# Kernel tuning notes

Hardware: AMD Instinct MI355X
Metric: run time of the kernel (lower is better)

Reference implementation:

```python
import jax, jax.numpy as jnp
import numpy as np
from jax import lax

N_NODES = 100000
N_EDGES = 1600000
NUM_GRAPHS = 2000
F_IN = 64
HIDDEN = 64
NUM_LAYERS = 3
K = 7
NUM_CLASSES = 10


def setup_inputs() -> dict:
    key = jax.random.key(0)
    ks = jax.random.split(key, 16)
    x = jax.random.normal(ks[0], (N_NODES, F_IN), jnp.float32)
    edge_index = jax.random.randint(ks[1], (2, N_EDGES), 0, N_NODES)
    batch = jnp.sort(jax.random.randint(ks[2], (N_NODES,), 0, NUM_GRAPHS))
    s = 1.0 / np.sqrt(HIDDEN)
    p = lambda k_, sh: jax.random.uniform(k_, sh, jnp.float32, -s, s)
    return dict(
        x=x, edge_index=edge_index, batch=batch,
        W1l=p(ks[3], (F_IN, HIDDEN)), b1=p(ks[4], (HIDDEN,)), W1r=p(ks[5], (F_IN, HIDDEN)),
        W2l=p(ks[6], (HIDDEN, HIDDEN)), b2=p(ks[7], (HIDDEN,)), W2r=p(ks[8], (HIDDEN, HIDDEN)),
        W3l=p(ks[9], (HIDDEN, HIDDEN)), b3=p(ks[10], (HIDDEN,)), W3r=p(ks[11], (HIDDEN, HIDDEN)),
        conv1d_w=p(ks[12], (32, HIDDEN, NUM_LAYERS)), conv1d_b=jnp.zeros((32,), jnp.float32),
        lin1_w=p(ks[13], (32 * (K - NUM_LAYERS + 1), HIDDEN)), lin1_b=jnp.zeros((HIDDEN,), jnp.float32),
        lin2_w=p(ks[14], (HIDDEN, NUM_CLASSES)), lin2_b=jnp.zeros((NUM_CLASSES,), jnp.float32),
    )


def _sage(x, src, dst, Wl, b, Wr):
    # PyG SAGEConv (aggr='mean'): lin_l(mean_j x_j) + lin_r(x_i); lin_l carries the bias.
    n = x.shape[0]
    msum = jax.ops.segment_sum(x[src], dst, num_segments=n)          # [N, D] gather+scatter
    cnt = jax.ops.segment_sum(jnp.ones((src.shape[0],), x.dtype), dst, num_segments=n)
    mean = msum / jnp.maximum(cnt, 1.0)[:, None]
    return mean @ Wl + b + x @ Wr


def _sort_pool(x, batch, num_graphs, k):
    # SortAggregation: per graph, sort nodes descending by last feature channel,
    # keep top-k, zero-pad short graphs, flatten to [B, k*D].
    N, D = x.shape
    perm = jnp.lexsort((-x[:, -1], batch))  # primary: graph id, secondary: desc last channel
    sb = batch[perm]
    counts = jax.ops.segment_sum(jnp.ones((N,), jnp.int32), batch, num_segments=num_graphs)
    starts = jnp.concatenate([jnp.zeros((1,), jnp.int32), jnp.cumsum(counts)[:-1]])
    rank = jnp.arange(N, dtype=jnp.int32) - starts[sb]
    valid = rank < k
    b_idx = jnp.where(valid, sb, num_graphs)  # route overflow nodes to dummy row
    r_idx = jnp.where(valid, rank, 0)
    out = jnp.zeros((num_graphs + 1, k, D), x.dtype).at[b_idx, r_idx].set(x[perm])
    return out[:num_graphs].reshape(num_graphs, k * D)


def reference(x, edge_index, batch, W1l, b1, W1r, W2l, b2, W2r, W3l, b3, W3r,
              conv1d_w, conv1d_b, lin1_w, lin1_b, lin2_w, lin2_b):
    src, dst = edge_index[0], edge_index[1]
    h = jax.nn.relu(_sage(x, src, dst, W1l, b1, W1r))
    h = jax.nn.relu(_sage(h, src, dst, W2l, b2, W2r))
    h = jax.nn.relu(_sage(h, src, dst, W3l, b3, W3r))
    g = _sort_pool(h, batch, NUM_GRAPHS, K)                       # [B, K*H]
    g = g.reshape(NUM_GRAPHS, K, HIDDEN).transpose(0, 2, 1)       # [B, H, K]
    c = lax.conv_general_dilated(g, conv1d_w, (1,), 'VALID',
                                 dimension_numbers=('NCH', 'OIH', 'NCH'))
    c = jax.nn.relu(c + conv1d_b[None, :, None])                  # [B, 32, K-ks+1]
    flat = c.reshape(NUM_GRAPHS, -1)
    h1 = jax.nn.relu(flat @ lin1_w + lin1_b)                      # dropout = identity (eval)
    logits = h1 @ lin2_w + lin2_b
    return jax.nn.log_softmax(logits, axis=-1)
```

## Files before the change

### kernel.cpp

```cpp
#include <hip/hip_runtime.h>
#include <hip/hip_bf16.h>

#define NN 100000
#define NE 1600000
#define NG 2000
#define KTOP 7

#define BNODES 128
#define NBKT 782
#define EPB 8192
#define NL1B 196
#define L2CAP 4096

#define GEMM_BLOCKS 768
#define NTILES 1563
#define SMEM_FLOATS (64 * 68 + 2 * 64 * 64)

#define ACC4(A, V) do { A.x += V.x; A.y += V.y; A.z += V.z; A.w += V.w; } while (0)
#define ACC4P(A, U, W) do { A.x += U.x + W.x; A.y += U.y + W.y; \
                            A.z += U.z + W.z; A.w += U.w + W.w; } while (0)

__device__ __forceinline__ void agg_node(const float* __restrict__ XLp, const int* __restrict__ ce,
        int s, int e, int fo, float4& a0, float4& a1, float4& a2, float4& a3) {
    int a = s;
    for (; a + 2 <= e; a += 2) {
        const float4* p0 = (const float4*)(XLp + ((size_t)ce[a] << 6) + fo);
        const float4* p1 = (const float4*)(XLp + ((size_t)ce[a + 1] << 6) + fo);
        float4 u0 = p0[0], u1 = p0[1], u2 = p0[2], u3 = p0[3];
        float4 w0 = p1[0], w1 = p1[1], w2 = p1[2], w3 = p1[3];
        ACC4P(a0, u0, w0); ACC4P(a1, u1, w1); ACC4P(a2, u2, w2); ACC4P(a3, u3, w3);
    }
    if (a < e) {
        const float4* p0 = (const float4*)(XLp + ((size_t)ce[a] << 6) + fo);
        float4 u0 = p0[0], u1 = p0[1], u2 = p0[2], u3 = p0[3];
        ACC4(a0, u0); ACC4(a1, u1); ACC4(a2, u2); ACC4(a3, u3);
    }
}

__device__ __forceinline__ void relu_mean_res(float inv, const float4* tp,
        float4& h0, float4& h1, float4& h2, float4& h3) {
    float4 t0 = tp[0], t1 = tp[1], t2 = tp[2], t3 = tp[3];
    h0.x = fmaxf(h0.x * inv + t0.x, 0.f); h0.y = fmaxf(h0.y * inv + t0.y, 0.f);
    h0.z = fmaxf(h0.z * inv + t0.z, 0.f); h0.w = fmaxf(h0.w * inv + t0.w, 0.f);
    h1.x = fmaxf(h1.x * inv + t1.x, 0.f); h1.y = fmaxf(h1.y * inv + t1.y, 0.f);
    h1.z = fmaxf(h1.z * inv + t1.z, 0.f); h1.w = fmaxf(h1.w * inv + t1.w, 0.f);
    h2.x = fmaxf(h2.x * inv + t2.x, 0.f); h2.y = fmaxf(h2.y * inv + t2.y, 0.f);
    h2.z = fmaxf(h2.z * inv + t2.z, 0.f); h2.w = fmaxf(h2.w * inv + t2.w, 0.f);
    h3.x = fmaxf(h3.x * inv + t3.x, 0.f); h3.y = fmaxf(h3.y * inv + t3.y, 0.f);
    h3.z = fmaxf(h3.z * inv + t3.z, 0.f); h3.w = fmaxf(h3.w * inv + t3.w, 0.f);
}

#define FMA4C(av, B, acc) do { \
    acc[0] = fmaf(av, B.x, acc[0]); acc[1] = fmaf(av, B.y, acc[1]); \
    acc[2] = fmaf(av, B.z, acc[2]); acc[3] = fmaf(av, B.w, acc[3]); } while (0)

__device__ __forceinline__ void gemm_tile(const float* As, const float* Bl, const float* Br,
        int n0, int ty4, int tx4, float b0, float b1v, float b2v, float b3v,
        float* __restrict__ XL, float* __restrict__ T,
        float* __restrict__ kc_out, float* __restrict__ tc_out) {
    float accl[4][4] = {{0.f}}, accr[4][4] = {{0.f}};
    for (int kc = 0; kc < 64; kc += 4) {
        float4 Av[4], L[4], R[4];
        #pragma unroll
        for (int i = 0; i < 4; ++i) Av[i] = *(const float4*)&As[(ty4 + i) * 68 + kc];
        #pragma unroll
        for (int j = 0; j < 4; ++j) {
            L[j] = *(const float4*)&Bl[(kc + j) * 64 + tx4];
            R[j] = *(const float4*)&Br[(kc + j) * 64 + tx4];
        }
        #pragma unroll
        for (int i = 0; i < 4; ++i) {
            FMA4C(Av[i].x, L[0], accl[i]); FMA4C(Av[i].y, L[1], accl[i]);
            FMA4C(Av[i].z, L[2], accl[i]); FMA4C(Av[i].w, L[3], accl[i]);
            FMA4C(Av[i].x, R[0], accr[i]); FMA4C(Av[i].y, R[1], accr[i]);
            FMA4C(Av[i].z, R[2], accr[i]); FMA4C(Av[i].w, R[3], accr[i]);
        }
    }
    #pragma unroll
    for (int i = 0; i < 4; ++i) {
        int g = n0 + ty4 + i;
        if (g < NN) {
            *(float4*)&XL[(size_t)g * 64 + tx4] =
                make_float4(accl[i][0], accl[i][1], accl[i][2], accl[i][3]);
            *(float4*)&T[(size_t)g * 64 + tx4] =
                make_float4(accr[i][0] + b0, accr[i][1] + b1v, accr[i][2] + b2v, accr[i][3] + b3v);
            if (kc_out && tx4 == 60) {
                kc_out[g] = accl[i][3];
                tc_out[g] = accr[i][3] + b3v;
            }
        }
    }
}

__device__ __forceinline__ void stage_weights(float* Bl, float* Br,
        const float* __restrict__ Wl, const float* __restrict__ Wr, int t) {
    #pragma unroll
    for (int q = 0; q < 4; ++q) {
        int idx = t + q * 256;
        ((float4*)Bl)[idx] = ((const float4*)Wl)[idx];
        ((float4*)Br)[idx] = ((const float4*)Wr)[idx];
    }
}

__device__ __forceinline__ void gemm_body(int bid, int nblocks, float* smem,
        const float* __restrict__ X, const float* __restrict__ Wl,
        const float* __restrict__ Wr, const float* __restrict__ bias,
        float* __restrict__ XL, float* __restrict__ T) {
    float* As = smem;
    float* Bl = smem + 64 * 68;
    float* Br = Bl + 64 * 64;
    int t = threadIdx.x;
    stage_weights(Bl, Br, Wl, Wr, t);
    int ty4 = (t >> 4) * 4, tx4 = (t & 15) * 4;
    float b0 = bias[tx4 + 0], b1v = bias[tx4 + 1], b2v = bias[tx4 + 2], b3v = bias[tx4 + 3];
    for (int tile = bid; tile < NTILES; tile += nblocks) {
        int n0 = tile * 64;
        #pragma unroll
        for (int q = 0; q < 4; ++q) {
            int f = t + q * 256;
            int node = f >> 4, seg = f & 15;
            int g = n0 + node;
            float4 v = make_float4(0.f, 0.f, 0.f, 0.f);
            if (g < NN) v = *(const float4*)&X[(size_t)g * 64 + seg * 4];
            *(float4*)&As[node * 68 + seg * 4] = v;
        }
        __syncthreads();
        gemm_tile(As, Bl, Br, n0, ty4, tx4, b0, b1v, b2v, b3v, XL, T, nullptr, nullptr);
        __syncthreads();
    }
}

__global__ __launch_bounds__(256) void k_aggemm(const float* __restrict__ XL_in,
        float* __restrict__ T, const int* __restrict__ ptr, const int* __restrict__ ce,
        const float* __restrict__ Wl, const float* __restrict__ Wr,
        const float* __restrict__ bias, float* __restrict__ XL_out,
        float* __restrict__ kc_out, float* __restrict__ tc_out) {
    __shared__ float smem[SMEM_FLOATS];
    float* As = smem;
    float* Bl = smem + 64 * 68;
    float* Br = Bl + 64 * 64;
    int t = threadIdx.x;
    stage_weights(Bl, Br, Wl, Wr, t);
    int node_l = t >> 2;
    int fo = (t & 3) * 16;
    int ty4 = (t >> 4) * 4, tx4 = (t & 15) * 4;
    float b0 = bias[tx4 + 0], b1v = bias[tx4 + 1], b2v = bias[tx4 + 2], b3v = bias[tx4 + 3];
    for (int tile = blockIdx.x; tile < NTILES; tile += GEMM_BLOCKS) {
        int n0 = tile * 64;
        int i = n0 + node_l;
        float4 h0 = make_float4(0.f, 0.f, 0.f, 0.f), h1 = h0, h2 = h0, h3 = h0;
        if (i < NN) {
            int s = ptr[i], e = ptr[i + 1];
            agg_node(XL_in, ce, s, e, fo, h0, h1, h2, h3);
            float inv = 1.f / fmaxf((float)(e - s), 1.f);
            relu_mean_res(inv, (const float4*)(T + ((size_t)i << 6) + fo), h0, h1, h2, h3);
        }
        float* dst = &As[node_l * 68 + fo];
        ((float4*)dst)[0] = h0; ((float4*)dst)[1] = h1;
        ((float4*)dst)[2] = h2; ((float4*)dst)[3] = h3;
        __syncthreads();
        gemm_tile(As, Bl, Br, n0, ty4, tx4, b0, b1v, b2v, b3v, XL_out, T, kc_out, tc_out);
        __syncthreads();
    }
}

__global__ __launch_bounds__(256) void k_key(const float* __restrict__ keycol,
        const float* __restrict__ tcol, const int* __restrict__ ptr,
        const int* __restrict__ ce, float* __restrict__ key) {
    int i = blockIdx.x * 256 + threadIdx.x;
    if (i >= NN) return;
    int s = ptr[i], e = ptr[i + 1];
    float acc = 0.f;
    int a = s;
    for (; a + 2 <= e; a += 2) acc += keycol[ce[a]] + keycol[ce[a + 1]];
    if (a < e) acc += keycol[ce[a]];
    float inv = 1.f / fmaxf((float)(e - s), 1.f);
    key[i] = fmaxf(acc * inv + tcol[i], 0.f);
}

__global__ __launch_bounds__(256) void k_topk(const float* __restrict__ key,
        const int* __restrict__ gstart, int* __restrict__ idx7, int G) {
    int wv = threadIdx.x >> 6, lane = threadIdx.x & 63;
    int b = blockIdx.x * 4 + wv;
    if (b >= G) return;
    int s = gstart[b], e = gstart[b + 1];
    float pk = 3.4e38f; int pi = -1;
    for (int r = 0; r < KTOP; ++r) {
        float bk = -1.f; int bi = -1;
        for (int i = s + lane; i < e; i += 64) {
            float k = key[i];
            bool elig = (k < pk) || (k == pk && i > pi);
            if (elig && (k > bk || (k == bk && (unsigned)i < (unsigned)bi))) { bk = k; bi = i; }
        }
        #pragma unroll
        for (int off = 1; off < 64; off <<= 1) {
            float ok = __shfl_xor(bk, off);
            int   oi = __shfl_xor(bi, off);
            if (ok > bk || (ok == bk && (unsigned)oi < (unsigned)bi)) { bk = ok; bi = oi; }
        }
        if (lane == 0) idx7[b * KTOP + r] = bi;
        pk = bk; pi = bi;
    }
}

__global__ __launch_bounds__(256) void k_aggW(const float* __restrict__ XL_in,
        const float* __restrict__ T, const int* __restrict__ ptr, const int* __restrict__ ce,
        const int* __restrict__ idx7, float* __restrict__ H3W) {
    int t = threadIdx.x;
    int j = blockIdx.x * 64 + (t >> 2);
    int fo = (t & 3) * 16;
    if (j >= NG * KTOP) return;
    int i = idx7[j];
    float4 h0 = make_float4(0.f, 0.f, 0.f, 0.f), h1 = h0, h2 = h0, h3 = h0;
    if (i >= 0) {
        int s = ptr[i], e = ptr[i + 1];
        agg_node(XL_in, ce, s, e, fo, h0, h1, h2, h3);
        float inv = 1.f / fmaxf((float)(e - s), 1.f);
        relu_mean_res(inv, (const float4*)(T + ((size_t)i << 6) + fo), h0, h1, h2, h3);
    }
    float4* dst = (float4*)(H3W + (size_t)j * 64 + fo);
    dst[0] = h0; dst[1] = h1; dst[2] = h2; dst[3] = h3;
}

__global__ __launch_bounds__(256) void k_front(const float* __restrict__ X,
        const float* __restrict__ Wl, const float* __restrict__ Wr,
        const float* __restrict__ bias, float* __restrict__ XL, float* __restrict__ T,
        const int* __restrict__ edst, int* __restrict__ bh,
        const int* __restrict__ bat, int* __restrict__ gstart) {
    __shared__ float smem[SMEM_FLOATS];
    int bid = blockIdx.x, t = threadIdx.x;
    if (bid < GEMM_BLOCKS) {
        gemm_body(bid, GEMM_BLOCKS, smem, X, Wl, Wr, bias, XL, T);
    } else if (bid < GEMM_BLOCKS + NL1B) {
        int bk = bid - GEMM_BLOCKS;
        int* h = (int*)smem;
        for (int q = t; q < NBKT; q += 256) h[q] = 0;
        __syncthreads();
        int e0 = bk * EPB, e1 = min(e0 + EPB, NE);
        for (int e = e0 + t; e < e1; e += 256) atomicAdd(&h[edst[e] >> 7], 1);
        __syncthreads();
        for (int q = t; q < NBKT; q += 256) bh[bk * NBKT + q] = h[q];
    } else {
        int g = (bid - GEMM_BLOCKS - NL1B) * 256 + t;
        if (g <= NG) {
            int lo = 0, hi = NN;
            while (lo < hi) { int mid = (lo + hi) >> 1; if (bat[mid] < g) lo = mid + 1; else hi = mid; }
            gstart[g] = lo;
        }
    }
}

__global__ void k_colscan(int* __restrict__ bh, int* __restrict__ btot) {
    __shared__ int carry;
    int b = blockIdx.x, t = threadIdx.x;
    if (t == 0) carry = 0;
    __syncthreads();
    for (int base = 0; base < NL1B; base += 64) {
        int idx = base + t;
        int v = (idx < NL1B) ? bh[idx * NBKT + b] : 0;
        int x = v;
        #pragma unroll
        for (int off = 1; off < 64; off <<= 1) {
            int y = __shfl_up(x, off);
            if (t >= off) x += y;
        }
        int c = carry;
        if (idx < NL1B) bh[idx * NBKT + b] = c + x - v;
        __syncthreads();
        if (t == 63) carry = c + x;
        __syncthreads();
    }
    if (t == 0) btot[b] = carry;
}

__global__ void k_btscan(const int* __restrict__ btot, int* __restrict__ bstart) {
    __shared__ int s[1024];
    int t = threadIdx.x;
    int v = (t < NBKT) ? btot[t] : 0;
    s[t] = v; __syncthreads();
    for (int off = 1; off < 1024; off <<= 1) {
        int y = (t >= off) ? s[t - off] : 0;
        __syncthreads();
        s[t] += y;
        __syncthreads();
    }
    if (t < NBKT) bstart[t] = s[t] - v;
    if (t == NBKT - 1) bstart[NBKT] = s[t];
}

__global__ __launch_bounds__(256) void k_bscatter(const int* __restrict__ esrc,
        const int* __restrict__ edst, const int* __restrict__ bh,
        const int* __restrict__ bstart, int* __restrict__ ebuf) {
    __shared__ int cur[NBKT];
    int t = threadIdx.x, bk = blockIdx.x;
    for (int q = t; q < NBKT; q += 256) cur[q] = bstart[q] + bh[bk * NBKT + q];
    __syncthreads();
    int e0 = bk * EPB, e1 = min(e0 + EPB, NE);
    for (int e = e0 + t; e < e1; e += 256) {
        int d = edst[e], s = esrc[e];
        int pos = atomicAdd(&cur[d >> 7], 1);
        ebuf[pos] = s | ((d & 127) << 20);
    }
}

__global__ __launch_bounds__(128) void k_bbuild(const int* __restrict__ ebuf,
        const int* __restrict__ bstart, int* __restrict__ ce, int* __restrict__ ptr) {
    __shared__ int lord[L2CAP];
    __shared__ int cnt[BNODES], sc[BNODES], cursor[BNODES];
    int b = blockIdx.x, t = threadIdx.x;
    int base = bstart[b], nb = bstart[b + 1] - base;
    cnt[t] = 0;
    __syncthreads();
    for (int j = t; j < nb; j += 128) atomicAdd(&cnt[ebuf[base + j] >> 20], 1);
    __syncthreads();
    int v = cnt[t]; sc[t] = v; __syncthreads();
    for (int off = 1; off < 128; off <<= 1) {
        int y = (t >= off) ? sc[t - off] : 0;
        __syncthreads();
        sc[t] += y;
        __syncthreads();
    }
    int segend = sc[t], segstart = sc[t] - v;
    cursor[t] = segstart;
    __syncthreads();
    bool fits = (nb <= L2CAP);
    for (int j = t; j < nb; j += 128) {
        int pv = ebuf[base + j];
        int node = pv >> 20;
        int pos = atomicAdd(&cursor[node], 1);
        if (fits) lord[pos] = pv & 0xFFFFF;
        else ce[base + pos] = pv & 0xFFFFF;
    }
    __syncthreads();
    if (fits) {
        for (int a = segstart + 1; a < segend; ++a) {
            int val = lord[a]; int j = a - 1;
            while (j >= segstart && lord[j] > val) { lord[j + 1] = lord[j]; --j; }
            lord[j + 1] = val;
        }
        __syncthreads();
        for (int j = t; j < nb; j += 128) ce[base + j] = lord[j];
    } else {
        for (int a = segstart + 1; a < segend; ++a) {
            int val = ce[base + a]; int j = a - 1;
            while (j >= segstart && ce[base + j] > val) { ce[base + j + 1] = ce[base + j]; --j; }
            ce[base + j + 1] = val;
        }
    }
    int node = b * BNODES + t;
    if (node <= NN) ptr[node] = base + segstart;
}

__global__ __launch_bounds__(256) void k_head(const float* __restrict__ H3W,
        const float* __restrict__ cw, const float* __restrict__ cb,
        const float* __restrict__ l1w, const float* __restrict__ l1b,
        const float* __restrict__ l2w, const float* __restrict__ l2b,
        float* __restrict__ out, int G) {
    __shared__ float sw[32 * 64 * 3];
    __shared__ float s2w[64 * 10];
    __shared__ float sg[4][KTOP][64];
    __shared__ float sflat[4][160];
    __shared__ float sh1[4][64];
    __shared__ float slog[4][10];
    int t = threadIdx.x;
    for (int q = t; q < 32 * 64 * 3; q += 256) sw[q] = cw[q];
    for (int q = t; q < 640; q += 256) s2w[q] = l2w[q];
    int wv = t >> 6, lane = t & 63;
    int b = blockIdx.x * 4 + wv;
    for (int r = 0; r < KTOP; ++r)
        sg[wv][r][lane] = H3W[(size_t)(b * KTOP + r) * 64 + lane];
    __syncthreads();
    for (int idx = lane; idx < 160; idx += 64) {
        int o = idx / 5, p = idx % 5;
        float acc = cb[o];
        #pragma unroll
        for (int dt = 0; dt < 3; ++dt) {
            const float* wrow = &sw[(o * 64) * 3 + dt];
            const float* grow = &sg[wv][p + dt][0];
            for (int i = 0; i < 64; ++i) acc = fmaf(wrow[i * 3], grow[i], acc);
        }
        sflat[wv][idx] = fmaxf(acc, 0.f);
    }
    __syncthreads();
    {
        float acc = l1b[lane];
        for (int k = 0; k < 160; ++k) acc = fmaf(sflat[wv][k], l1w[k * 64 + lane], acc);
        sh1[wv][lane] = fmaxf(acc, 0.f);
    }
    __syncthreads();
    if (lane < 10) {
        float acc = l2b[lane];
        for (int k = 0; k < 64; ++k) acc = fmaf(sh1[wv][k], s2w[k * 10 + lane], acc);
        slog[wv][lane] = acc;
    }
    __syncthreads();
    if (lane < 10) {
        float m = -3.4e38f;
        for (int j = 0; j < 10; ++j) m = fmaxf(m, slog[wv][j]);
        float ssum = 0.f;
        for (int j = 0; j < 10; ++j) ssum += expf(slog[wv][j] - m);
        out[b * 10 + lane] = slog[wv][lane] - m - logf(ssum);
    }
}

extern "C" void kernel_launch(void* const* d_in, const int* in_sizes, int n_in,
                              void* d_out, int out_size, void* d_ws, size_t ws_size,
                              hipStream_t stream) {
    const float* x   = (const float*)d_in[0];
    const int*   ei  = (const int*)d_in[1];
    const int*   bat = (const int*)d_in[2];
    const float* W1l = (const float*)d_in[3], *b1 = (const float*)d_in[4], *W1r = (const float*)d_in[5];
    const float* W2l = (const float*)d_in[6], *b2 = (const float*)d_in[7], *W2r = (const float*)d_in[8];
    const float* W3l = (const float*)d_in[9], *b3 = (const float*)d_in[10], *W3r = (const float*)d_in[11];
    const float* cw  = (const float*)d_in[12], *cb  = (const float*)d_in[13];
    const float* l1w = (const float*)d_in[14], *l1b = (const float*)d_in[15];
    const float* l2w = (const float*)d_in[16], *l2b = (const float*)d_in[17];
    float* out = (float*)d_out;
    const int* esrc = ei;
    const int* edst = ei + NE;

    char* w = (char*)d_ws;
    size_t off = 0;
    auto take = [&](size_t bytes) { void* p = w + off; off = (off + bytes + 255) & ~(size_t)255; return p; };
    int*   bh      = (int*)take((size_t)NL1B * NBKT * 4);
    int*   btot    = (int*)take((size_t)NBKT * 4);
    int*   bstart  = (int*)take((size_t)(NBKT + 1) * 4);
    int*   gstart  = (int*)take((size_t)(NG + 1) * 4);
    int*   idx7    = (int*)take((size_t)NG * KTOP * 4);
    int*   ebuf    = (int*)take((size_t)NE * 4);
    int*   csr_ptr = (int*)take((size_t)(NN + 1) * 4);
    int*   csr_e   = (int*)take((size_t)NE * 4);
    float* XLa     = (float*)take((size_t)NN * 64 * 4);
    float* XLb     = (float*)take((size_t)NN * 64 * 4);
    float* T       = (float*)take((size_t)NN * 64 * 4);
    float* keycol  = (float*)take((size_t)NN * 4);
    float* tcol    = (float*)take((size_t)NN * 4);
    float* key     = (float*)take((size_t)NN * 4);
    float* H3W     = (float*)take((size_t)NG * KTOP * 64 * 4);

    k_front<<<GEMM_BLOCKS + NL1B + 8, 256, 0, stream>>>(x, W1l, W1r, b1, XLa, T,
                                                        edst, bh, bat, gstart);
    k_colscan<<<NBKT, 64, 0, stream>>>(bh, btot);
    k_btscan <<<1, 1024, 0, stream>>>(btot, bstart);
    k_bscatter<<<NL1B, 256, 0, stream>>>(esrc, edst, bh, bstart, ebuf);
    k_bbuild <<<NBKT, 128, 0, stream>>>(ebuf, bstart, csr_e, csr_ptr);

    k_aggemm<<<GEMM_BLOCKS, 256, 0, stream>>>(XLa, T, csr_ptr, csr_e, W2l, W2r, b2, XLb,
                                              nullptr, nullptr);
    k_aggemm<<<GEMM_BLOCKS, 256, 0, stream>>>(XLb, T, csr_ptr, csr_e, W3l, W3r, b3, XLa,
                                              keycol, tcol);

    k_key <<<(NN + 255) / 256, 256, 0, stream>>>(keycol, tcol, csr_ptr, csr_e, key);
    k_topk<<<(NG + 3) / 4, 256, 0, stream>>>(key, gstart, idx7, NG);
    k_aggW<<<(NG * KTOP + 63) / 64, 256, 0, stream>>>(XLa, T, csr_ptr, csr_e, idx7, H3W);
    k_head<<<NG / 4, 256, 0, stream>>>(H3W, cw, cb, l1w, l1b, l2w, l2b, out, NG);
}
```

Baseline: 330.1 us.

## Fuse key, top-k, gather and head into one tail kernel; drop bucket-scan kernel

Merges the key computation, per-graph top-k selection, aggregation of the selected nodes and the classifier head into a single per-graph kernel. Keys are cached in shared memory up to a capacity and recomputed beyond it. The bucket histogram is stored transposed so the column scan reads contiguously. The separate bucket-total scan kernel is removed: the scatter kernel does the exclusive scan itself, and the build kernel reduces its own prefix. This cuts four launches and the intermediate key and H3W buffers. In exchange it adds redundant prefix work in every block and serial per-graph work in the tail.

```diff
diff --git a/kernel.cpp b/kernel.cpp
--- a/kernel.cpp
+++ b/kernel.cpp
@@ -5,6 +5,7 @@
 #define NE 1600000
 #define NG 2000
 #define KTOP 7
+#define KCAP 192
 
 #define BNODES 128
 #define NBKT 782
@@ -48,6 +49,18 @@
     h2.z = fmaxf(h2.z * inv + t2.z, 0.f); h2.w = fmaxf(h2.w * inv + t2.w, 0.f);
     h3.x = fmaxf(h3.x * inv + t3.x, 0.f); h3.y = fmaxf(h3.y * inv + t3.y, 0.f);
     h3.z = fmaxf(h3.z * inv + t3.z, 0.f); h3.w = fmaxf(h3.w * inv + t3.w, 0.f);
+}
+
+__device__ __forceinline__ float compute_key(int i, const float* __restrict__ keycol,
+        const float* __restrict__ tcol, const int* __restrict__ ptr,
+        const int* __restrict__ ce) {
+    int s = ptr[i], e = ptr[i + 1];
+    float acc = 0.f;
+    int a = s;
+    for (; a + 2 <= e; a += 2) acc += keycol[ce[a]] + keycol[ce[a + 1]];
+    if (a < e) acc += keycol[ce[a]];
+    float inv = 1.f / fmaxf((float)(e - s), 1.f);
+    return fmaxf(acc * inv + tcol[i], 0.f);
 }
 
 #define FMA4C(av, B, acc) do { \
@@ -164,68 +177,10 @@
     }
 }
 
-__global__ __launch_bounds__(256) void k_key(const float* __restrict__ keycol,
-        const float* __restrict__ tcol, const int* __restrict__ ptr,
-        const int* __restrict__ ce, float* __restrict__ key) {
-    int i = blockIdx.x * 256 + threadIdx.x;
-    if (i >= NN) return;
-    int s = ptr[i], e = ptr[i + 1];
-    float acc = 0.f;
-    int a = s;
-    for (; a + 2 <= e; a += 2) acc += keycol[ce[a]] + keycol[ce[a + 1]];
-    if (a < e) acc += keycol[ce[a]];
-    float inv = 1.f / fmaxf((float)(e - s), 1.f);
-    key[i] = fmaxf(acc * inv + tcol[i], 0.f);
-}
-
-__global__ __launch_bounds__(256) void k_topk(const float* __restrict__ key,
-        const int* __restrict__ gstart, int* __restrict__ idx7, int G) {
-    int wv = threadIdx.x >> 6, lane = threadIdx.x & 63;
-    int b = blockIdx.x * 4 + wv;
-    if (b >= G) return;
-    int s = gstart[b], e = gstart[b + 1];
-    float pk = 3.4e38f; int pi = -1;
-    for (int r = 0; r < KTOP; ++r) {
-        float bk = -1.f; int bi = -1;
-        for (int i = s + lane; i < e; i += 64) {
-            float k = key[i];
-            bool elig = (k < pk) || (k == pk && i > pi);
-            if (elig && (k > bk || (k == bk && (unsigned)i < (unsigned)bi))) { bk = k; bi = i; }
-        }
-        #pragma unroll
-        for (int off = 1; off < 64; off <<= 1) {
-            float ok = __shfl_xor(bk, off);
-            int   oi = __shfl_xor(bi, off);
-            if (ok > bk || (ok == bk && (unsigned)oi < (unsigned)bi)) { bk = ok; bi = oi; }
-        }
-        if (lane == 0) idx7[b * KTOP + r] = bi;
-        pk = bk; pi = bi;
-    }
-}
-
-__global__ __launch_bounds__(256) void k_aggW(const float* __restrict__ XL_in,
-        const float* __restrict__ T, const int* __restrict__ ptr, const int* __restrict__ ce,
-        const int* __restrict__ idx7, float* __restrict__ H3W) {
-    int t = threadIdx.x;
-    int j = blockIdx.x * 64 + (t >> 2);
-    int fo = (t & 3) * 16;
-    if (j >= NG * KTOP) return;
-    int i = idx7[j];
-    float4 h0 = make_float4(0.f, 0.f, 0.f, 0.f), h1 = h0, h2 = h0, h3 = h0;
-    if (i >= 0) {
-        int s = ptr[i], e = ptr[i + 1];
-        agg_node(XL_in, ce, s, e, fo, h0, h1, h2, h3);
-        float inv = 1.f / fmaxf((float)(e - s), 1.f);
-        relu_mean_res(inv, (const float4*)(T + ((size_t)i << 6) + fo), h0, h1, h2, h3);
-    }
-    float4* dst = (float4*)(H3W + (size_t)j * 64 + fo);
-    dst[0] = h0; dst[1] = h1; dst[2] = h2; dst[3] = h3;
-}
-
 __global__ __launch_bounds__(256) void k_front(const float* __restrict__ X,
         const float* __restrict__ Wl, const float* __restrict__ Wr,
         const float* __restrict__ bias, float* __restrict__ XL, float* __restrict__ T,
-        const int* __restrict__ edst, int* __restrict__ bh,
+        const int* __restrict__ edst, int* __restrict__ bh_t,
         const int* __restrict__ bat, int* __restrict__ gstart) {
     __shared__ float smem[SMEM_FLOATS];
     int bid = blockIdx.x, t = threadIdx.x;
@@ -239,7 +194,7 @@
         int e0 = bk * EPB, e1 = min(e0 + EPB, NE);
         for (int e = e0 + t; e < e1; e += 256) atomicAdd(&h[edst[e] >> 7], 1);
         __syncthreads();
-        for (int q = t; q < NBKT; q += 256) bh[bk * NBKT + q] = h[q];
+        for (int q = t; q < NBKT; q += 256) bh_t[q * NL1B + bk] = h[q];
     } else {
         int g = (bid - GEMM_BLOCKS - NL1B) * 256 + t;
         if (g <= NG) {
@@ -250,14 +205,14 @@
     }
 }
 
-__global__ void k_colscan(int* __restrict__ bh, int* __restrict__ btot) {
+__global__ void k_colscan(int* __restrict__ bh_t, int* __restrict__ btot) {
     __shared__ int carry;
     int b = blockIdx.x, t = threadIdx.x;
     if (t == 0) carry = 0;
     __syncthreads();
     for (int base = 0; base < NL1B; base += 64) {
         int idx = base + t;
-        int v = (idx < NL1B) ? bh[idx * NBKT + b] : 0;
+        int v = (idx < NL1B) ? bh_t[b * NL1B + idx] : 0;
         int x = v;
         #pragma unroll
         for (int off = 1; off < 64; off <<= 1) {
@@ -265,7 +220,7 @@
             if (t >= off) x += y;
         }
         int c = carry;
-        if (idx < NL1B) bh[idx * NBKT + b] = c + x - v;
+        if (idx < NL1B) bh_t[b * NL1B + idx] = c + x - v;
         __syncthreads();
         if (t == 63) carry = c + x;
         __syncthreads();
@@ -273,27 +228,31 @@
     if (t == 0) btot[b] = carry;
 }
 
-__global__ void k_btscan(const int* __restrict__ btot, int* __restrict__ bstart) {
-    __shared__ int s[1024];
-    int t = threadIdx.x;
-    int v = (t < NBKT) ? btot[t] : 0;
-    s[t] = v; __syncthreads();
-    for (int off = 1; off < 1024; off <<= 1) {
-        int y = (t >= off) ? s[t - off] : 0;
-        __syncthreads();
-        s[t] += y;
-        __syncthreads();
-    }
-    if (t < NBKT) bstart[t] = s[t] - v;
-    if (t == NBKT - 1) bstart[NBKT] = s[t];
-}
-
 __global__ __launch_bounds__(256) void k_bscatter(const int* __restrict__ esrc,
-        const int* __restrict__ edst, const int* __restrict__ bh,
-        const int* __restrict__ bstart, int* __restrict__ ebuf) {
+        const int* __restrict__ edst, const int* __restrict__ bh_t,
+        const int* __restrict__ btot, int* __restrict__ ebuf) {
+    __shared__ int sbt[1024];
+    __shared__ int ssum[256];
     __shared__ int cur[NBKT];
     int t = threadIdx.x, bk = blockIdx.x;
-    for (int q = t; q < NBKT; q += 256) cur[q] = bstart[q] + bh[bk * NBKT + q];
+    for (int q = t; q < 1024; q += 256) sbt[q] = (q < NBKT) ? btot[q] : 0;
+    __syncthreads();
+    int base = t * 4;
+    int a0 = sbt[base], a1 = sbt[base + 1], a2 = sbt[base + 2], a3 = sbt[base + 3];
+    int s1 = a0 + a1, s2 = s1 + a2, s3 = s2 + a3;
+    ssum[t] = s3;
+    __syncthreads();
+    for (int off = 1; off < 256; off <<= 1) {
+        int y = (t >= off) ? ssum[t - off] : 0;
+        __syncthreads();
+        ssum[t] += y;
+        __syncthreads();
+    }
+    int prev = (t > 0) ? ssum[t - 1] : 0;
+    sbt[base] = prev; sbt[base + 1] = prev + a0;
+    sbt[base + 2] = prev + s1; sbt[base + 3] = prev + s2;
+    __syncthreads();
+    for (int q = t; q < NBKT; q += 256) cur[q] = sbt[q] + bh_t[q * NL1B + bk];
     __syncthreads();
     int e0 = bk * EPB, e1 = min(e0 + EPB, NE);
     for (int e = e0 + t; e < e1; e += 256) {
@@ -304,11 +263,21 @@
 }
 
 __global__ __launch_bounds__(128) void k_bbuild(const int* __restrict__ ebuf,
-        const int* __restrict__ bstart, int* __restrict__ ce, int* __restrict__ ptr) {
+        const int* __restrict__ btot, int* __restrict__ ce, int* __restrict__ ptr) {
     __shared__ int lord[L2CAP];
     __shared__ int cnt[BNODES], sc[BNODES], cursor[BNODES];
+    __shared__ int red[128];
     int b = blockIdx.x, t = threadIdx.x;
-    int base = bstart[b], nb = bstart[b + 1] - base;
+    int part = 0;
+    for (int j = t; j < b; j += 128) part += btot[j];
+    red[t] = part;
+    __syncthreads();
+    for (int off = 64; off >= 1; off >>= 1) {
+        if (t < off) red[t] += red[t + off];
+        __syncthreads();
+    }
+    int base = red[0];
+    int nb = btot[b];
     cnt[t] = 0;
     __syncthreads();
     for (int j = t; j < nb; j += 128) atomicAdd(&cnt[ebuf[base + j] >> 20], 1);
@@ -351,7 +320,10 @@
     if (node <= NN) ptr[node] = base + segstart;
 }
 
-__global__ __launch_bounds__(256) void k_head(const float* __restrict__ H3W,
+__global__ __launch_bounds__(256) void k_tail(const int* __restrict__ gstart,
+        const float* __restrict__ keycol, const float* __restrict__ tcol,
+        const int* __restrict__ ptr, const int* __restrict__ ce,
+        const float* __restrict__ XLa, const float* __restrict__ T,
         const float* __restrict__ cw, const float* __restrict__ cb,
         const float* __restrict__ l1w, const float* __restrict__ l1b,
         const float* __restrict__ l2w, const float* __restrict__ l2b,
@@ -362,13 +334,53 @@
     __shared__ float sflat[4][160];
     __shared__ float sh1[4][64];
     __shared__ float slog[4][10];
+    __shared__ float skey[4][KCAP];
+    __shared__ int   widx[4][KTOP];
     int t = threadIdx.x;
     for (int q = t; q < 32 * 64 * 3; q += 256) sw[q] = cw[q];
     for (int q = t; q < 640; q += 256) s2w[q] = l2w[q];
     int wv = t >> 6, lane = t & 63;
     int b = blockIdx.x * 4 + wv;
-    for (int r = 0; r < KTOP; ++r)
-        sg[wv][r][lane] = H3W[(size_t)(b * KTOP + r) * 64 + lane];
+    int s = gstart[b], e = gstart[b + 1];
+    int cnt = e - s;
+    for (int base = 0; base < cnt; base += 64) {
+        int o = base + lane;
+        if (o < cnt && o < KCAP) skey[wv][o] = compute_key(s + o, keycol, tcol, ptr, ce);
+    }
+    {
+        float pk = 3.4e38f; int pi = -1;
+        for (int r = 0; r < KTOP; ++r) {
+            float bk = -1.f; int bi = -1;
+            for (int o = lane; o < cnt; o += 64) {
+                int i = s + o;
+                float k = (o < KCAP) ? skey[wv][o] : compute_key(i, keycol, tcol, ptr, ce);
+                bool elig = (k < pk) || (k == pk && i > pi);
+                if (elig && (k > bk || (k == bk && (unsigned)i < (unsigned)bi))) { bk = k; bi = i; }
+            }
+            #pragma unroll
+            for (int off = 1; off < 64; off <<= 1) {
+                float ok = __shfl_xor(bk, off);
+                int   oi = __shfl_xor(bi, off);
+                if (ok > bk || (ok == bk && (unsigned)oi < (unsigned)bi)) { bk = ok; bi = oi; }
+            }
+            if (lane == 0) widx[wv][r] = bi;
+            pk = bk; pi = bi;
+        }
+    }
+    if (lane < 28) {
+        int r = lane >> 2, fo = (lane & 3) * 16;
+        int i = widx[wv][r];
+        float4 h0 = make_float4(0.f, 0.f, 0.f, 0.f), h1 = h0, h2 = h0, h3 = h0;
+        if (i >= 0) {
+            int s2 = ptr[i], e2 = ptr[i + 1];
+            agg_node(XLa, ce, s2, e2, fo, h0, h1, h2, h3);
+            float inv = 1.f / fmaxf((float)(e2 - s2), 1.f);
+            relu_mean_res(inv, (const float4*)(T + ((size_t)i << 6) + fo), h0, h1, h2, h3);
+        }
+        float* dstp = &sg[wv][r][fo];
+        ((float4*)dstp)[0] = h0; ((float4*)dstp)[1] = h1;
+        ((float4*)dstp)[2] = h2; ((float4*)dstp)[3] = h3;
+    }
     __syncthreads();
     for (int idx = lane; idx < 160; idx += 64) {
         int o = idx / 5, p = idx % 5;
@@ -422,11 +434,9 @@
     char* w = (char*)d_ws;
     size_t off = 0;
     auto take = [&](size_t bytes) { void* p = w + off; off = (off + bytes + 255) & ~(size_t)255; return p; };
-    int*   bh      = (int*)take((size_t)NL1B * NBKT * 4);
+    int*   bh_t    = (int*)take((size_t)NBKT * NL1B * 4);
     int*   btot    = (int*)take((size_t)NBKT * 4);
-    int*   bstart  = (int*)take((size_t)(NBKT + 1) * 4);
     int*   gstart  = (int*)take((size_t)(NG + 1) * 4);
-    int*   idx7    = (int*)take((size_t)NG * KTOP * 4);
     int*   ebuf    = (int*)take((size_t)NE * 4);
     int*   csr_ptr = (int*)take((size_t)(NN + 1) * 4);
     int*   csr_e   = (int*)take((size_t)NE * 4);
@@ -435,23 +445,18 @@
     float* T       = (float*)take((size_t)NN * 64 * 4);
     float* keycol  = (float*)take((size_t)NN * 4);
     float* tcol    = (float*)take((size_t)NN * 4);
-    float* key     = (float*)take((size_t)NN * 4);
-    float* H3W     = (float*)take((size_t)NG * KTOP * 64 * 4);
 
     k_front<<<GEMM_BLOCKS + NL1B + 8, 256, 0, stream>>>(x, W1l, W1r, b1, XLa, T,
-                                                        edst, bh, bat, gstart);
-    k_colscan<<<NBKT, 64, 0, stream>>>(bh, btot);
-    k_btscan <<<1, 1024, 0, stream>>>(btot, bstart);
-    k_bscatter<<<NL1B, 256, 0, stream>>>(esrc, edst, bh, bstart, ebuf);
-    k_bbuild <<<NBKT, 128, 0, stream>>>(ebuf, bstart, csr_e, csr_ptr);
+                                                        edst, bh_t, bat, gstart);
+    k_colscan<<<NBKT, 64, 0, stream>>>(bh_t, btot);
+    k_bscatter<<<NL1B, 256, 0, stream>>>(esrc, edst, bh_t, btot, ebuf);
+    k_bbuild <<<NBKT, 128, 0, stream>>>(ebuf, btot, csr_e, csr_ptr);
 
     k_aggemm<<<GEMM_BLOCKS, 256, 0, stream>>>(XLa, T, csr_ptr, csr_e, W2l, W2r, b2, XLb,
                                               nullptr, nullptr);
     k_aggemm<<<GEMM_BLOCKS, 256, 0, stream>>>(XLb, T, csr_ptr, csr_e, W3l, W3r, b3, XLa,
                                               keycol, tcol);
 
-    k_key <<<(NN + 255) / 256, 256, 0, stream>>>(keycol, tcol, csr_ptr, csr_e, key);
-    k_topk<<<(NG + 3) / 4, 256, 0, stream>>>(key, gstart, idx7, NG);
-    k_aggW<<<(NG * KTOP + 63) / 64, 256, 0, stream>>>(XLa, T, csr_ptr, csr_e, idx7, H3W);
-    k_head<<<NG / 4, 256, 0, stream>>>(H3W, cw, cb, l1w, l1b, l2w, l2b, out, NG);
-}
+    k_tail<<<NG / 4, 256, 0, stream>>>(gstart, keycol, tcol, csr_ptr, csr_e, XLa, T,
+                                       cw, cb, l1w, l1b, l2w, l2b, out, NG);
+}
```

New measurement: 318.6 us, median of 2. 1.04x faster.
